# Optimization experiments

Hardware: AMD Instinct MI355X
Metric: run time of the kernel (lower is better)

## Reference

```python
import jax, jax.numpy as jnp
import numpy as np

B, S, H = 4, 2048, 1024
HEADS = 16
DFF = 4 * H
EPS = 1e-12


def _layer_norm(x, w, b):
    mu = jnp.mean(x, axis=-1, keepdims=True)
    var = jnp.mean(jnp.square(x - mu), axis=-1, keepdims=True)
    return (x - mu) * jax.lax.rsqrt(var + EPS) * w + b


def setup_inputs() -> dict:
    key = jax.random.key(0)
    ks = jax.random.split(key, 12)
    sc = 0.02
    return {
        "input": jax.random.normal(ks[0], (B, S, H), dtype=jnp.float32),
        "input_mask": jnp.zeros((B, 1, 1, S), dtype=jnp.float32),
        "norm_w": jnp.ones((H,), jnp.float32),
        "norm_b": jnp.zeros((H,), jnp.float32),
        "qkv_w": sc * jax.random.normal(ks[1], (H, 3 * H), jnp.float32),
        "qkv_b": jnp.zeros((3 * H,), jnp.float32),
        "attn_ow": sc * jax.random.normal(ks[2], (H, H), jnp.float32),
        "attn_ob": jnp.zeros((H,), jnp.float32),
        "attn_nw": jnp.ones((H,), jnp.float32),
        "attn_nb": jnp.zeros((H,), jnp.float32),
        "inter_w": sc * jax.random.normal(ks[3], (H, DFF), jnp.float32),
        "inter_b": jnp.zeros((DFF,), jnp.float32),
        "output_w": sc * jax.random.normal(ks[4], (DFF, H), jnp.float32),
        "output_b": jnp.zeros((H,), jnp.float32),
    }


def reference(input, input_mask, norm_w, norm_b, qkv_w, qkv_b, attn_ow, attn_ob,
              attn_nw, attn_nb, inter_w, inter_b, output_w, output_b):
    b, s, h = input.shape
    hd = h // HEADS
    # pre-LN + fused QKV projection (qkv_func)
    x_ln = _layer_norm(input, norm_w, norm_b)
    qkv = x_ln @ qkv_w + qkv_b                      # [b, s, 3h]
    qkv = qkv.reshape(b, s, 3, HEADS, hd)
    q, k, v = qkv[:, :, 0], qkv[:, :, 1], qkv[:, :, 2]   # [b, s, heads, hd]
    # scaled dot-product attention (flash_attn equivalent, non-causal)
    scale = 1.0 / jnp.sqrt(jnp.float32(hd))
    scores = jnp.einsum('bqnd,bknd->bnqk', q, k) * scale  # [b, heads, s, s]
    scores = scores + input_mask                           # additive mask
    probs = jax.nn.softmax(scores, axis=-1)
    ctx = jnp.einsum('bnqk,bknd->bqnd', probs, v).reshape(b, s, h)
    # attention output projection + residual (mlp_func first half)
    attn_out = ctx @ attn_ow + attn_ob + input
    # post-attention LN + FFN (GELU) + residual
    y = _layer_norm(attn_out, attn_nw, attn_nb)
    y = jax.nn.gelu(y @ inter_w + inter_b, approximate=False)
    return y @ output_w + output_b + attn_out
```

## Files before the change

### kernel.cpp

```cpp
#include <hip/hip_runtime.h>
#include <math.h>

typedef __bf16 bf16_t;
typedef bf16_t bf16x8 __attribute__((ext_vector_type(8)));
typedef bf16_t bf16x4 __attribute__((ext_vector_type(4)));
typedef float f32x4 __attribute__((ext_vector_type(4)));
typedef float f32x16 __attribute__((ext_vector_type(16)));

#define BB 4
#define SS 2048
#define HD1 1024
#define NH 16
#define DFF_ 4096

__device__ __forceinline__ void gload_lds16(const bf16_t* g, bf16_t* l) {
  __builtin_amdgcn_global_load_lds(
      (const __attribute__((address_space(1))) void*)g,
      (__attribute__((address_space(3))) void*)l, 16, 0, 0);
}

__device__ __forceinline__ unsigned pack2_bf16(float a, float b) {
  unsigned r;
  asm("v_cvt_pk_bf16_f32 %0, %1, %2" : "=v"(r) : "v"(a), "v"(b));
  return r;
}

__device__ __forceinline__ float block_reduce_sum(float v, float* red) {
  const int lane = threadIdx.x & 63;
  const int wid = threadIdx.x >> 6;
#pragma unroll
  for (int off = 32; off > 0; off >>= 1) v += __shfl_down(v, off, 64);
  if (lane == 0) red[wid] = v;
  __syncthreads();
  float s = red[0] + red[1] + red[2] + red[3];
  __syncthreads();
  return s;
}

__global__ __launch_bounds__(256) void ln_kernel(const float* __restrict__ x,
                                                 const float* __restrict__ w,
                                                 const float* __restrict__ bv,
                                                 bf16_t* __restrict__ out) {
  __shared__ float red[4];
  const size_t row = blockIdx.x;
  const float4 xv = *(const float4*)(x + row * HD1 + threadIdx.x * 4);
  float s = xv.x + xv.y + xv.z + xv.w;
  s = block_reduce_sum(s, red);
  const float mu = s * (1.0f / HD1);
  float4 d;
  d.x = xv.x - mu; d.y = xv.y - mu; d.z = xv.z - mu; d.w = xv.w - mu;
  float sq = d.x * d.x + d.y * d.y + d.z * d.z + d.w * d.w;
  sq = block_reduce_sum(sq, red);
  const float rs = rsqrtf(sq * (1.0f / HD1) + 1e-12f);
  const float4 wv = *(const float4*)(w + threadIdx.x * 4);
  const float4 bb = *(const float4*)(bv + threadIdx.x * 4);
  bf16x4 o;
  o[0] = (bf16_t)(d.x * rs * wv.x + bb.x);
  o[1] = (bf16_t)(d.y * rs * wv.y + bb.y);
  o[2] = (bf16_t)(d.z * rs * wv.z + bb.z);
  o[3] = (bf16_t)(d.w * rs * wv.w + bb.w);
  *(bf16x4*)(out + row * HD1 + threadIdx.x * 4) = o;
}

__global__ __launch_bounds__(256) void wt_kernel(const float* __restrict__ W,
                                                 bf16_t* __restrict__ Wt,
                                                 int K, int N) {
  __shared__ bf16_t T[32][33];
  const int t = threadIdx.x;
  const int n0 = blockIdx.x * 32, k0 = blockIdx.y * 32;
  const int a = t >> 5, c = t & 31;
#pragma unroll
  for (int i = 0; i < 4; ++i) {
    const int kl = a + i * 8;
    T[kl][c] = (bf16_t)W[(size_t)(k0 + kl) * N + n0 + c];
  }
  __syncthreads();
#pragma unroll
  for (int i = 0; i < 4; ++i) {
    const int nl = a + i * 8;
    Wt[(size_t)(n0 + nl) * K + k0 + c] = T[c][nl];
  }
}

__global__ __launch_bounds__(256) void vtrans_kernel(const bf16_t* __restrict__ qkv,
                                                     bf16_t* __restrict__ Vt) {
  __shared__ bf16_t T[256 * 66];
  const int t = threadIdx.x;
  const int s0 = blockIdx.x * 256;
  const int head = blockIdx.y, b = blockIdx.z;
  const int rr = t >> 3, dc = (t & 7) * 8;
#pragma unroll
  for (int p = 0; p < 8; ++p) {
    const int s = rr + p * 32;
    const bf16x8 v = *(const bf16x8*)(
        qkv + (size_t)(b * SS + s0 + s) * 3072 + 2048 + head * 64 + dc);
    *(bf16x8*)&T[s * 66 + dc] = v;
  }
  __syncthreads();
  const int dd = t >> 3;
  const int sw = (t & 7) * 8;
#pragma unroll
  for (int p = 0; p < 2; ++p) {
    const int d = dd + p * 32;
    bf16_t* dst = Vt + ((size_t)(b * NH + head) * 64 + d) * SS + s0;
#pragma unroll
    for (int j = 0; j < 4; ++j) {
      bf16x8 o;
#pragma unroll
      for (int e = 0; e < 8; ++e) o[e] = T[(sw + j * 64 + e) * 66 + d];
      *(bf16x8*)(dst + sw + j * 64) = o;
    }
  }
}

template <int EPI, bool OBF>
__global__ __launch_bounds__(256) void gemm_bf16(
    const bf16_t* __restrict__ A, const bf16_t* __restrict__ Wt,
    const float* __restrict__ bias, const float* __restrict__ R,
    void* __restrict__ Cout, int M, int N, int K) {
  __shared__ __align__(16) char smem[65536];
  bf16_t* As = (bf16_t*)smem;
  bf16_t* Bs = (bf16_t*)(smem + 32768);
  const int tid = threadIdx.x;
  const int lane = tid & 63;
  const int w = tid >> 6;
  const int wm = (w >> 1) * 64, wn = (w & 1) * 64;
  const int l31 = lane & 31;
  const int h = lane >> 5;

  const int gx = gridDim.x;
  int id = blockIdx.x + gx * blockIdx.y;
  const int cpx = (gx * gridDim.y) >> 3;
  id = (id & 7) * cpx + (id >> 3);
  const int m0 = (id / gx) * 128;
  const int n0 = (id % gx) * 128;

  const int lrow = tid >> 3;
  const int lcol = (((tid & 7) ^ ((tid >> 3) & 7)) * 8);
  const bf16_t* Ag = A + (size_t)(m0 + lrow) * K + lcol;
  const bf16_t* Bg = Wt + (size_t)(n0 + lrow) * K + lcol;
  const size_t rstride = (size_t)32 * K;

#pragma unroll
  for (int c = 0; c < 4; ++c) {
    gload_lds16(Ag + c * rstride, As + c * 2048 + w * 512);
    gload_lds16(Bg + c * rstride, Bs + c * 2048 + w * 512);
  }

  const int NT = K >> 6;
  f32x16 acc[2][2] = {};

  for (int t = 0; t < NT; ++t) {
    const int cur = t & 1;
    __syncthreads();
    if (t + 1 < NT) {
      const bf16_t* Agn = Ag + (size_t)(t + 1) * 64;
      const bf16_t* Bgn = Bg + (size_t)(t + 1) * 64;
      bf16_t* Ad = As + (cur ^ 1) * 8192;
      bf16_t* Bd = Bs + (cur ^ 1) * 8192;
#pragma unroll
      for (int c = 0; c < 4; ++c) {
        gload_lds16(Agn + c * rstride, Ad + c * 2048 + w * 512);
        gload_lds16(Bgn + c * rstride, Bd + c * 2048 + w * 512);
      }
    }
    const bf16_t* Ab = As + cur * 8192;
    const bf16_t* Bb = Bs + cur * 8192;
    bf16x8 af[4][2], bfr[4][2];
#pragma unroll
    for (int ks = 0; ks < 4; ++ks) {
      const int ch = ((2 * ks + h) ^ (l31 & 7)) * 8;
#pragma unroll
      for (int i = 0; i < 2; ++i)
        af[ks][i] = *(const bf16x8*)(Ab + (wm + i * 32 + l31) * 64 + ch);
#pragma unroll
      for (int j = 0; j < 2; ++j)
        bfr[ks][j] = *(const bf16x8*)(Bb + (wn + j * 32 + l31) * 64 + ch);
    }
#pragma unroll
    for (int ks = 0; ks < 4; ++ks)
#pragma unroll
      for (int i = 0; i < 2; ++i)
#pragma unroll
        for (int j = 0; j < 2; ++j)
          acc[i][j] = __builtin_amdgcn_mfma_f32_32x32x16_bf16(
              af[ks][i], bfr[ks][j], acc[i][j], 0, 0, 0);
  }

  if (OBF) {
    __syncthreads();
    float* Cs = (float*)smem;
#pragma unroll
    for (int j = 0; j < 2; ++j) {
      const int col = wn + j * 32 + l31;
      const float bj = bias[n0 + col];
#pragma unroll
      for (int i = 0; i < 2; ++i)
#pragma unroll
        for (int r = 0; r < 16; ++r) {
          float v = acc[i][j][r] + bj;
          if (EPI == 1)
            v = 0.5f * v * (1.0f + erff(v * 0.70710678118654752440f));
          const int row = wm + i * 32 + (r & 3) + 8 * (r >> 2) + 4 * h;
          const int q = (((col >> 2) ^ (row & 7)) << 2);
          Cs[row * 128 + q + (col & 3)] = v;
        }
    }
    __syncthreads();
    bf16_t* Cb = (bf16_t*)Cout;
#pragma unroll
    for (int p = 0; p < 16; ++p) {
      const int idx = p * 256 + tid;
      const int row = idx >> 5, c4 = idx & 31;
      const int q = (((c4) ^ (row & 7)) << 2);
      const f32x4 v = *(const f32x4*)(Cs + row * 128 + q);
      bf16x4 o;
      o[0] = (bf16_t)v[0]; o[1] = (bf16_t)v[1];
      o[2] = (bf16_t)v[2]; o[3] = (bf16_t)v[3];
      *(bf16x4*)(Cb + (size_t)(m0 + row) * N + n0 + c4 * 4) = o;
    }
  } else {
    float* Cf = (float*)Cout;
#pragma unroll
    for (int j = 0; j < 2; ++j) {
      const int gn = n0 + wn + j * 32 + l31;
      const float bj = bias[gn];
#pragma unroll
      for (int i = 0; i < 2; ++i) {
#pragma unroll
        for (int r = 0; r < 16; ++r) {
          const int gm = m0 + wm + i * 32 + (r & 3) + 8 * (r >> 2) + 4 * h;
          float v = acc[i][j][r] + bj;
          if (EPI == 2) v += R[(size_t)gm * N + gn];
          Cf[(size_t)gm * N + gn] = v;
        }
      }
    }
  }
}

__global__ __launch_bounds__(256, 3) void attn_kernel(
    const bf16_t* __restrict__ qkv, const bf16_t* __restrict__ Vt,
    const float* __restrict__ mask, bf16_t* __restrict__ ctx) {
  __shared__ __align__(16) bf16_t K_lds[64 * 72];
  __shared__ __align__(16) bf16_t Vt_lds[64 * 72];
  const int tid = threadIdx.x;
  const int lane = tid & 63;
  const int w = tid >> 6;
  const int l31 = lane & 31;
  const int h = lane >> 5;

  const int p = blockIdx.x;
  const int xcd = p & 7;
  const int c = p >> 3;
  const int j = c & 15;
  const int g = (c >> 4) * 8 + xcd;
  const int b = g >> 4;
  const int head = g & 15;
  const int q0 = j * 128;

  const int qrow = q0 + w * 32 + l31;

  bf16x8 qf[4];
  {
    const bf16_t* qp = qkv + (size_t)(b * SS + qrow) * 3072 + head * 64 + 8 * h;
#pragma unroll
    for (int ks = 0; ks < 4; ++ks) qf[ks] = *(const bf16x8*)(qp + 16 * ks);
  }

  const int srow = tid >> 2;
  const int scol = (tid & 3) * 16;
  const bf16_t* kp0 =
      qkv + (size_t)(b * SS + srow) * 3072 + 1024 + head * 64 + scol;
  const bf16_t* vp0 = Vt + ((size_t)(b * NH + head) * 64 + srow) * SS + scol;

  bf16x8 kr0 = *(const bf16x8*)kp0;
  bf16x8 kr1 = *(const bf16x8*)(kp0 + 8);
  bf16x8 vr0 = *(const bf16x8*)vp0;
  bf16x8 vr1 = *(const bf16x8*)(vp0 + 8);

  float m = -3.0e38f, l = 0.0f;
  f32x16 cacc0 = {};
  f32x16 cacc1 = {};

  for (int kv0 = 0; kv0 < SS; kv0 += 64) {
    __syncthreads();
    *(bf16x8*)(K_lds + srow * 72 + scol) = kr0;
    *(bf16x8*)(K_lds + srow * 72 + scol + 8) = kr1;
    *(bf16x8*)(Vt_lds + srow * 72 + scol) = vr0;
    *(bf16x8*)(Vt_lds + srow * 72 + scol + 8) = vr1;
    if (kv0 + 64 < SS) {
      const bf16_t* kp = kp0 + (size_t)(kv0 + 64) * 3072;
      const bf16_t* vp = vp0 + (kv0 + 64);
      kr0 = *(const bf16x8*)kp;
      kr1 = *(const bf16x8*)(kp + 8);
      vr0 = *(const bf16x8*)vp;
      vr1 = *(const bf16x8*)(vp + 8);
    }
    float4 mv[8];
#pragma unroll
    for (int k2 = 0; k2 < 8; ++k2)
      mv[k2] = *(const float4*)(mask + (size_t)b * SS + kv0 + 8 * k2 + 4 * h);
    __syncthreads();

    f32x16 sacc0 = {};
    f32x16 sacc1 = {};
#pragma unroll
    for (int ks = 0; ks < 4; ++ks) {
      const bf16x8 kf0 = *(const bf16x8*)(K_lds + l31 * 72 + 16 * ks + 8 * h);
      const bf16x8 kf1 =
          *(const bf16x8*)(K_lds + (l31 + 32) * 72 + 16 * ks + 8 * h);
      sacc0 = __builtin_amdgcn_mfma_f32_32x32x16_bf16(kf0, qf[ks], sacc0, 0, 0, 0);
      sacc1 = __builtin_amdgcn_mfma_f32_32x32x16_bf16(kf1, qf[ks], sacc1, 0, 0, 0);
    }

    float ps[32];
    float tmax = -3.0e38f;
#pragma unroll
    for (int r = 0; r < 16; ++r) {
      const float s0 = sacc0[r] * 0.125f + mv[(r >> 2)][r & 3];
      const float s1 = sacc1[r] * 0.125f + mv[(r >> 2) + 4][r & 3];
      ps[r] = s0;
      ps[16 + r] = s1;
      tmax = fmaxf(tmax, fmaxf(s0, s1));
    }
    tmax = fmaxf(tmax, __shfl_xor(tmax, 32, 64));
    if (__any(tmax > m + 8.0f)) {
      const float mnew = fmaxf(m, tmax);
      const float sc = __expf(m - mnew);
      m = mnew;
      l *= sc;
#pragma unroll
      for (int r = 0; r < 16; ++r) {
        const float scr = __shfl(sc, (r & 3) + 8 * (r >> 2) + 4 * h, 64);
        cacc0[r] *= scr;
        cacc1[r] *= scr;
      }
    }
    float ls = 0.0f;
#pragma unroll
    for (int i = 0; i < 32; ++i) {
      ps[i] = __expf(ps[i] - m);
      ls += ps[i];
    }
    l += ls + __shfl_xor(ls, 32, 64);

    unsigned pw0[8], pw1[8];
#pragma unroll
    for (int k = 0; k < 8; ++k) {
      const int base = (k >> 2) * 16 + (k & 3) * 4;
      pw0[k] = pack2_bf16(ps[base + 0], ps[base + 1]);
      pw1[k] = pack2_bf16(ps[base + 2], ps[base + 3]);
    }
#pragma unroll
    for (int t = 0; t < 4; ++t) {
      const unsigned e0 = h ? pw0[2 * t] : pw0[2 * t + 1];
      const unsigned e1 = h ? pw1[2 * t] : pw1[2 * t + 1];
      const unsigned o0 = (unsigned)__shfl_xor((int)e0, 32, 64);
      const unsigned o1 = (unsigned)__shfl_xor((int)e1, 32, 64);
      const unsigned a0 = h ? pw0[2 * t + 1] : pw0[2 * t];
      const unsigned a1 = h ? pw1[2 * t + 1] : pw1[2 * t];
      union { unsigned u[4]; bf16x8 v; } pu;
      pu.u[0] = h ? o0 : a0;
      pu.u[1] = h ? o1 : a1;
      pu.u[2] = h ? a0 : o0;
      pu.u[3] = h ? a1 : o1;
      const bf16x8 vf0 = *(const bf16x8*)(Vt_lds + l31 * 72 + 16 * t + 8 * h);
      const bf16x8 vf1 =
          *(const bf16x8*)(Vt_lds + (l31 + 32) * 72 + 16 * t + 8 * h);
      cacc0 = __builtin_amdgcn_mfma_f32_32x32x16_bf16(pu.v, vf0, cacc0, 0, 0, 0);
      cacc1 = __builtin_amdgcn_mfma_f32_32x32x16_bf16(pu.v, vf1, cacc1, 0, 0, 0);
    }
  }

  const float linv = 1.0f / l;
#pragma unroll
  for (int r = 0; r < 16; ++r) {
    const int rq = (r & 3) + 8 * (r >> 2) + 4 * h;
    const float li = __shfl(linv, rq, 64);
    const int grow = q0 + w * 32 + rq;
    bf16_t* op = ctx + (size_t)(b * SS + grow) * 1024 + head * 64 + l31;
    op[0] = (bf16_t)(cacc0[r] * li);
    op[32] = (bf16_t)(cacc1[r] * li);
  }
}

extern "C" void kernel_launch(void* const* d_in, const int* in_sizes, int n_in,
                              void* d_out, int out_size, void* d_ws, size_t ws_size,
                              hipStream_t stream) {
  const float* input    = (const float*)d_in[0];
  const float* mask     = (const float*)d_in[1];
  const float* norm_w   = (const float*)d_in[2];
  const float* norm_b   = (const float*)d_in[3];
  const float* qkv_w    = (const float*)d_in[4];
  const float* qkv_b    = (const float*)d_in[5];
  const float* attn_ow  = (const float*)d_in[6];
  const float* attn_ob  = (const float*)d_in[7];
  const float* attn_nw  = (const float*)d_in[8];
  const float* attn_nb  = (const float*)d_in[9];
  const float* inter_w  = (const float*)d_in[10];
  const float* inter_b  = (const float*)d_in[11];
  const float* output_w = (const float*)d_in[12];
  const float* output_b = (const float*)d_in[13];

  char* ws = (char*)d_ws;
  const size_t off_xln = 0;
  const size_t off_qkv = 16777216;
  const size_t off_vt  = 67108864;
  const size_t off_ctx = 83886080;
  const size_t off_ao  = 100663296;
  const size_t off_wq  = 134217728;
  const size_t off_wo  = 140509184;
  const size_t off_wi  = 142606336;
  const size_t off_w2  = 150994944;
  const size_t NEED    = 159383552;
  if (ws_size < NEED) return;

  bf16_t* x_ln  = (bf16_t*)(ws + off_xln);
  bf16_t* qkvb  = (bf16_t*)(ws + off_qkv);
  bf16_t* VtB   = (bf16_t*)(ws + off_vt);
  bf16_t* ctxb  = (bf16_t*)(ws + off_ctx);
  bf16_t* y_ln  = (bf16_t*)(ws + off_ctx);
  float*  a_out = (float*)(ws + off_ao);
  bf16_t* wq_t  = (bf16_t*)(ws + off_wq);
  bf16_t* wo_t  = (bf16_t*)(ws + off_wo);
  bf16_t* wi_t  = (bf16_t*)(ws + off_wi);
  bf16_t* w2_t  = (bf16_t*)(ws + off_w2);
  bf16_t* act   = (bf16_t*)(ws + off_xln);

  const int M = BB * SS;

  wt_kernel<<<dim3(3072 / 32, 1024 / 32), 256, 0, stream>>>(qkv_w, wq_t, 1024, 3072);
  wt_kernel<<<dim3(1024 / 32, 1024 / 32), 256, 0, stream>>>(attn_ow, wo_t, 1024, 1024);
  wt_kernel<<<dim3(4096 / 32, 1024 / 32), 256, 0, stream>>>(inter_w, wi_t, 1024, 4096);
  wt_kernel<<<dim3(1024 / 32, 4096 / 32), 256, 0, stream>>>(output_w, w2_t, 4096, 1024);

  ln_kernel<<<M, 256, 0, stream>>>(input, norm_w, norm_b, x_ln);
  gemm_bf16<0, true><<<dim3(3072 / 128, M / 128), 256, 0, stream>>>(
      x_ln, wq_t, qkv_b, nullptr, qkvb, M, 3072, 1024);
  vtrans_kernel<<<dim3(SS / 256, NH, BB), 256, 0, stream>>>(qkvb, VtB);
  attn_kernel<<<1024, 256, 0, stream>>>(qkvb, VtB, mask, ctxb);
  gemm_bf16<2, false><<<dim3(1024 / 128, M / 128), 256, 0, stream>>>(
      ctxb, wo_t, attn_ob, input, a_out, M, 1024, 1024);
  ln_kernel<<<M, 256, 0, stream>>>(a_out, attn_nw, attn_nb, y_ln);
  gemm_bf16<1, true><<<dim3(4096 / 128, M / 128), 256, 0, stream>>>(
      y_ln, wi_t, inter_b, nullptr, act, M, 4096, 1024);
  gemm_bf16<2, false><<<dim3(1024 / 128, M / 128), 256, 0, stream>>>(
      act, w2_t, output_b, a_out, (float*)d_out, M, 1024, 4096);
}
```

Before: 469.8 us.

## Widen GEMM tiles to 128x256 with 512 threads and triple-buffered LDS pipeline

The bf16 GEMM now uses 8 waves per block over a 128x256 output tile and keeps three LDS stages in flight. Explicit vmcnt waits replace full __syncthreads, so the next-next tile's loads overlap with the current tile's MFMAs. This reduces per-block B reloads and global-load latency stalls. The cost is 144KB of LDS per block, which limits occupancy to one block per CU, and grids with fewer blocks for the N=1024 GEMMs.

Measured after the change: 477.6 us. About the same (+1.7%).

```diff
diff --git a/kernel.cpp b/kernel.cpp
--- a/kernel.cpp
+++ b/kernel.cpp
@@ -113,18 +113,20 @@
   }
 }
 
+#define VM6 asm volatile("s_waitcnt vmcnt(6)" ::: "memory")
+#define VM0 asm volatile("s_waitcnt vmcnt(0)" ::: "memory")
+
 template <int EPI, bool OBF>
-__global__ __launch_bounds__(256) void gemm_bf16(
+__global__ __launch_bounds__(512) void gemm_bf16(
     const bf16_t* __restrict__ A, const bf16_t* __restrict__ Wt,
     const float* __restrict__ bias, const float* __restrict__ R,
     void* __restrict__ Cout, int M, int N, int K) {
-  __shared__ __align__(16) char smem[65536];
-  bf16_t* As = (bf16_t*)smem;
-  bf16_t* Bs = (bf16_t*)(smem + 32768);
+  __shared__ __align__(16) char smem[147456];
   const int tid = threadIdx.x;
   const int lane = tid & 63;
   const int w = tid >> 6;
-  const int wm = (w >> 1) * 64, wn = (w & 1) * 64;
+  const int wr = w >> 2, wc = w & 3;
+  const int wm = wr * 64, wn = wc * 64;
   const int l31 = lane & 31;
   const int h = lane >> 5;
 
@@ -133,39 +135,46 @@
   const int cpx = (gx * gridDim.y) >> 3;
   id = (id & 7) * cpx + (id >> 3);
   const int m0 = (id / gx) * 128;
-  const int n0 = (id % gx) * 128;
+  const int n0 = (id % gx) * 256;
 
   const int lrow = tid >> 3;
   const int lcol = (((tid & 7) ^ ((tid >> 3) & 7)) * 8);
   const bf16_t* Ag = A + (size_t)(m0 + lrow) * K + lcol;
   const bf16_t* Bg = Wt + (size_t)(n0 + lrow) * K + lcol;
-  const size_t rstride = (size_t)32 * K;
-
-#pragma unroll
-  for (int c = 0; c < 4; ++c) {
-    gload_lds16(Ag + c * rstride, As + c * 2048 + w * 512);
-    gload_lds16(Bg + c * rstride, Bs + c * 2048 + w * 512);
-  }
+  const size_t rs64 = (size_t)64 * K;
+
+  bf16_t* lds = (bf16_t*)smem;
+
+#define STAGE(BUF, T)                                                     \
+  do {                                                                    \
+    bf16_t* Ad = lds + (BUF)*24576 + w * 512;                             \
+    bf16_t* Bd = lds + (BUF)*24576 + 8192 + w * 512;                      \
+    const bf16_t* Agt = Ag + (size_t)(T)*64;                              \
+    const bf16_t* Bgt = Bg + (size_t)(T)*64;                              \
+    gload_lds16(Agt, Ad);                                                 \
+    gload_lds16(Agt + rs64, Ad + 4096);                                   \
+    gload_lds16(Bgt, Bd);                                                 \
+    gload_lds16(Bgt + rs64, Bd + 4096);                                   \
+    gload_lds16(Bgt + 2 * rs64, Bd + 8192);                               \
+    gload_lds16(Bgt + 3 * rs64, Bd + 12288);                              \
+  } while (0)
 
   const int NT = K >> 6;
+  STAGE(0, 0);
+  STAGE(1, 1);
+
   f32x16 acc[2][2] = {};
+  int cur = 0;
 
   for (int t = 0; t < NT; ++t) {
-    const int cur = t & 1;
-    __syncthreads();
-    if (t + 1 < NT) {
-      const bf16_t* Agn = Ag + (size_t)(t + 1) * 64;
-      const bf16_t* Bgn = Bg + (size_t)(t + 1) * 64;
-      bf16_t* Ad = As + (cur ^ 1) * 8192;
-      bf16_t* Bd = Bs + (cur ^ 1) * 8192;
-#pragma unroll
-      for (int c = 0; c < 4; ++c) {
-        gload_lds16(Agn + c * rstride, Ad + c * 2048 + w * 512);
-        gload_lds16(Bgn + c * rstride, Bd + c * 2048 + w * 512);
-      }
-    }
-    const bf16_t* Ab = As + cur * 8192;
-    const bf16_t* Bb = Bs + cur * 8192;
+    if (t + 1 < NT) { VM6; } else { VM0; }
+    __builtin_amdgcn_s_barrier();
+    if (t + 2 < NT) {
+      const int nb = cur == 0 ? 2 : (cur == 1 ? 0 : 1);
+      STAGE(nb, t + 2);
+    }
+    const bf16_t* Ab = lds + cur * 24576;
+    const bf16_t* Bb = Ab + 8192;
     bf16x8 af[4][2], bfr[4][2];
 #pragma unroll
     for (int ks = 0; ks < 4; ++ks) {
@@ -185,7 +194,9 @@
         for (int j = 0; j < 2; ++j)
           acc[i][j] = __builtin_amdgcn_mfma_f32_32x32x16_bf16(
               af[ks][i], bfr[ks][j], acc[i][j], 0, 0, 0);
-  }
+    cur = cur == 2 ? 0 : cur + 1;
+  }
+#undef STAGE
 
   if (OBF) {
     __syncthreads();
@@ -203,17 +214,17 @@
             v = 0.5f * v * (1.0f + erff(v * 0.70710678118654752440f));
           const int row = wm + i * 32 + (r & 3) + 8 * (r >> 2) + 4 * h;
           const int q = (((col >> 2) ^ (row & 7)) << 2);
-          Cs[row * 128 + q + (col & 3)] = v;
+          Cs[row * 256 + q + (col & 3)] = v;
         }
     }
     __syncthreads();
     bf16_t* Cb = (bf16_t*)Cout;
 #pragma unroll
     for (int p = 0; p < 16; ++p) {
-      const int idx = p * 256 + tid;
-      const int row = idx >> 5, c4 = idx & 31;
-      const int q = (((c4) ^ (row & 7)) << 2);
-      const f32x4 v = *(const f32x4*)(Cs + row * 128 + q);
+      const int idx = p * 512 + tid;
+      const int row = idx >> 6, c4 = idx & 63;
+      const int q = ((c4 ^ (row & 7)) << 2);
+      const f32x4 v = *(const f32x4*)(Cs + row * 256 + q);
       bf16x4 o;
       o[0] = (bf16_t)v[0]; o[1] = (bf16_t)v[1];
       o[2] = (bf16_t)v[2]; o[3] = (bf16_t)v[3];
@@ -436,15 +447,15 @@
   wt_kernel<<<dim3(1024 / 32, 4096 / 32), 256, 0, stream>>>(output_w, w2_t, 4096, 1024);
 
   ln_kernel<<<M, 256, 0, stream>>>(input, norm_w, norm_b, x_ln);
-  gemm_bf16<0, true><<<dim3(3072 / 128, M / 128), 256, 0, stream>>>(
+  gemm_bf16<0, true><<<dim3(3072 / 256, M / 128), 512, 0, stream>>>(
       x_ln, wq_t, qkv_b, nullptr, qkvb, M, 3072, 1024);
   vtrans_kernel<<<dim3(SS / 256, NH, BB), 256, 0, stream>>>(qkvb, VtB);
   attn_kernel<<<1024, 256, 0, stream>>>(qkvb, VtB, mask, ctxb);
-  gemm_bf16<2, false><<<dim3(1024 / 128, M / 128), 256, 0, stream>>>(
+  gemm_bf16<2, false><<<dim3(1024 / 256, M / 128), 512, 0, stream>>>(
       ctxb, wo_t, attn_ob, input, a_out, M, 1024, 1024);
   ln_kernel<<<M, 256, 0, stream>>>(a_out, attn_nw, attn_nb, y_ln);
-  gemm_bf16<1, true><<<dim3(4096 / 128, M / 128), 256, 0, stream>>>(
+  gemm_bf16<1, true><<<dim3(4096 / 256, M / 128), 512, 0, stream>>>(
       y_ln, wi_t, inter_b, nullptr, act, M, 4096, 1024);
-  gemm_bf16<2, false><<<dim3(1024 / 128, M / 128), 256, 0, stream>>>(
+  gemm_bf16<2, false><<<dim3(1024 / 256, M / 128), 512, 0, stream>>>(
       act, w2_t, output_b, a_out, (float*)d_out, M, 1024, 4096);
 }
```
